# Kernel optimization log

Hardware: AMD Instinct MI355X
Metric: run time of the kernel (lower is better)

The kernel has to match this reference:

```python
import jax, jax.numpy as jnp
import numpy as np

B, M, D, H, DH = 8, 1024, 768, 12, 64
R, RF, RW, DFF = 32, 384, 384, 3072
EPS = 1e-12  # BERT LayerNorm eps


def _ln(z, g, b):
    mu = jnp.mean(z, -1, keepdims=True)
    var = jnp.mean((z - mu) ** 2, -1, keepdims=True)
    return g * (z - mu) * jax.lax.rsqrt(var + EPS) + b


def setup_inputs() -> dict:
    ks = jax.random.split(jax.random.key(0), 20)
    n = lambda k, s: jax.random.normal(k, s, dtype=jnp.float32) * 0.02
    return {
        "x": jax.random.normal(ks[0], (B, M, D), dtype=jnp.float32),
        "mask": jnp.zeros((B, M), jnp.float32),  # additive attention mask
        "Pq": n(ks[1], (H, D, R)), "Vq": n(ks[2], (H, R, DH)), "bq": n(ks[3], (H, DH)),
        "Pk": n(ks[4], (H, D, R)), "Vk": n(ks[5], (H, R, DH)), "bk": n(ks[6], (H, DH)),
        "Pv": n(ks[7], (H, D, R)), "Vv": n(ks[8], (H, R, DH)), "bv": n(ks[9], (H, DH)),
        "Uo": n(ks[10], (D, RW)), "Vo": n(ks[11], (RW, D)), "bo_attn": n(ks[12], (D,)),
        "U1": n(ks[13], (D, RF)), "V1": n(ks[14], (RF, DFF)), "b1": n(ks[15], (DFF,)),
        "U2": n(ks[16], (DFF, RF)), "V2": n(ks[17], (RF, D)), "b2": n(ks[18], (D,)),
        "ln1_g": jnp.ones((D,), jnp.float32), "ln1_b": jnp.zeros((D,), jnp.float32),
        "ln2_g": jnp.ones((D,), jnp.float32), "ln2_b": jnp.zeros((D,), jnp.float32),
    }


def reference(x, mask, Pq, Vq, bq, Pk, Vk, bk, Pv, Vv, bv, Uo, Vo, bo_attn,
              U1, V1, b1, U2, V2, b2, ln1_g, ln1_b, ln2_g, ln2_b):
    Bx, Mx, dm = x.shape
    dh = dm // Pq.shape[0]
    scale = 1.0 / (dh ** 0.5)
    # low-rank per-head Q/K/V: x @ P (d->r) then @ V (r->dh), + per-head bias
    Q = jnp.einsum('bmd,hdr,hrk->bhmk', x, Pq, Vq) + bq[None, :, None, :]
    K = jnp.einsum('bmd,hdr,hrk->bhmk', x, Pk, Vk) + bk[None, :, None, :]
    V = jnp.einsum('bmd,hdr,hrk->bhmk', x, Pv, Vv) + bv[None, :, None, :]
    scores = jnp.einsum('bhmk,bhnk->bhmn', Q, K) * scale + mask[:, None, None, :]
    probs = jax.nn.softmax(scores, axis=-1)
    attn = jnp.einsum('bhmn,bhnk->bhmk', probs, V)
    attn = attn.transpose(0, 2, 1, 3).reshape(Bx, Mx, dm)  # (B, M, d_model)
    # low-rank attention output projection + residual + LN1
    x1 = _ln(x + (attn @ Uo) @ Vo + bo_attn, ln1_g, ln1_b)
    # low-rank FFN: GELU((x1 @ U1) @ V1 + b1) @ U2 @ V2 + b2 (BERT exact gelu)
    mid = x1 @ U1
    y = (jax.nn.gelu(mid @ V1 + b1, approximate=False) @ U2) @ V2 + b2
    return _ln(x1 + y, ln2_g, ln2_b)
```

## Files before the change

kernel.cpp:

```cpp
#include <hip/hip_runtime.h>
#include <cstddef>

#define D_MODEL 768
#define NHEAD   12
#define DHEAD   64
#define RANK    32
#define SEQ     1024
#define BATCH   8
#define BM      8192

typedef __attribute__((ext_vector_type(8))) short short8;
typedef __attribute__((ext_vector_type(4))) float floatx4;

__device__ inline ushort f2b(float f) {
  union { float f; unsigned u; } v; v.f = f;
  unsigned r = v.u + 0x7fffu + ((v.u >> 16) & 1u);
  return (ushort)(r >> 16);
}
__device__ inline float b2f(ushort h) {
  union { unsigned u; float f; } v; v.u = ((unsigned)h) << 16;
  return v.f;
}
__device__ inline unsigned pk2(float a, float b) {
  return ((__float_as_uint(b) + 0x8000u) & 0xffff0000u) |
         ((__float_as_uint(a) + 0x8000u) >> 16);
}
__device__ inline float fast_gelu(float x) {
  float z = 0.79788456080286536f * (x + 0.044715f * x * x * x);
  float e = __expf(2.f * z);
  float t = 1.f - 2.f / (e + 1.f);
  return 0.5f * x * (1.f + t);
}

__global__ __launch_bounds__(256) void f2b_kernel(
    const float* __restrict__ in, ushort* __restrict__ out, int n) {
  int i = (blockIdx.x * 256 + threadIdx.x) * 4;
  if (i >= n) return;
  float4 v = *(const float4*)(in + i);
  ushort4 o;
  o.x = f2b(v.x); o.y = f2b(v.y); o.z = f2b(v.z); o.w = f2b(v.w);
  *(ushort4*)(out + i) = o;
}

__global__ __launch_bounds__(256) void combine_qkv_kernel(
    const float* __restrict__ Pq, const float* __restrict__ Vq,
    const float* __restrict__ Pk, const float* __restrict__ Vk,
    const float* __restrict__ Pv, const float* __restrict__ Vv,
    ushort* __restrict__ Wt) {
  int which = blockIdx.y;
  const float* P  = which == 0 ? Pq : (which == 1 ? Pk : Pv);
  const float* Vw = which == 0 ? Vq : (which == 1 ? Vk : Vv);
  ushort* W = Wt + (size_t)which * D_MODEL * D_MODEL;
  int idx = blockIdx.x * 256 + threadIdx.x;
  if (idx >= D_MODEL * NHEAD * DHEAD) return;
  int c = idx / D_MODEL;
  int d = idx - c * D_MODEL;
  int h = c >> 6, k = c & 63;
  const float* p = P + ((size_t)h * D_MODEL + d) * RANK;
  const float* v = Vw + (size_t)h * RANK * DHEAD + k;
  float s = 0.f;
#pragma unroll
  for (int r = 0; r < RANK; r++) s += p[r] * v[(size_t)r * DHEAD];
  W[(size_t)c * D_MODEL + d] = f2b(s);
}

__global__ __launch_bounds__(256) void concat_bias_kernel(
    const float* __restrict__ bq, const float* __restrict__ bk,
    const float* __restrict__ bv, float* __restrict__ out) {
  int i = blockIdx.x * 256 + threadIdx.x;
  if (i >= 2304) return;
  out[i] = (i < 768) ? bq[i] : (i < 1536 ? bk[i - 768] : bv[i - 1536]);
}

__global__ __launch_bounds__(256) void prep_weights_kernel(
    const float* __restrict__ U1, const float* __restrict__ V1,
    const float* __restrict__ U2, const float* __restrict__ V2,
    const float* __restrict__ Vo, const float* __restrict__ Uo,
    ushort* __restrict__ U1t, ushort* __restrict__ V1t,
    ushort* __restrict__ U2t, ushort* __restrict__ V2t,
    ushort* __restrict__ VoT, ushort* __restrict__ Uob) {
  __shared__ float t[32][33];
  int blk = blockIdx.x;
  if (blk >= 3168) {
    int i = (blk - 3168) * 1024 + threadIdx.x * 4;
    float4 v = *(const float4*)(Uo + i);
    ushort4 o;
    o.x = f2b(v.x); o.y = f2b(v.y); o.z = f2b(v.z); o.w = f2b(v.w);
    *(ushort4*)(Uob + i) = o;
    return;
  }
  const float* in; ushort* out; int R, C, bx, by;
  if (blk < 288)       { in = U1; out = U1t; R = 768;  C = 384;  int i = blk;        bx = i % 12; by = i / 12; }
  else if (blk < 1440) { in = V1; out = V1t; R = 384;  C = 3072; int i = blk - 288;  bx = i % 96; by = i / 96; }
  else if (blk < 2592) { in = U2; out = U2t; R = 3072; C = 384;  int i = blk - 1440; bx = i % 12; by = i / 12; }
  else if (blk < 2880) { in = V2; out = V2t; R = 384;  C = 768;  int i = blk - 2592; bx = i % 24; by = i / 24; }
  else                 { in = Vo; out = VoT; R = 384;  C = 768;  int i = blk - 2880; bx = i % 24; by = i / 24; }
  int c0 = bx * 32, r0 = by * 32;
  int lx = threadIdx.x & 31, ly = threadIdx.x >> 5;
#pragma unroll
  for (int i = 0; i < 32; i += 8)
    t[ly + i][lx] = in[(size_t)(r0 + ly + i) * C + c0 + lx];
  __syncthreads();
#pragma unroll
  for (int i = 0; i < 32; i += 8)
    out[(size_t)(c0 + ly + i) * R + r0 + lx] = f2b(t[lx][ly + i]);
}

template <int OUTMODE, int BIAS, int GELU>
__global__ __launch_bounds__(256) void gemm_mfma_kernel(
    const ushort* __restrict__ A, const ushort* __restrict__ Bt,
    const float* __restrict__ bias, void* __restrict__ C,
    void* __restrict__ C2, void* __restrict__ C3,
    int M, int N, int K) {
  __shared__ __align__(16) ushort Als[128 * 32];
  __shared__ __align__(16) ushort Bls[128 * 32];
  const int tid  = threadIdx.x;
  const int lane = tid & 63;
  const int quad = lane >> 4, l16 = lane & 15;
  const int wu   = __builtin_amdgcn_readfirstlane(tid >> 6);
  const int wrow = (wu >> 1) * 64, wcol = (wu & 1) * 64;
  const int row0 = blockIdx.x * 128, col0 = blockIdx.y * 128;

  floatx4 acc[4][4] = {};

  for (int k0 = 0; k0 < K; k0 += 32) {
    __syncthreads();
#pragma unroll
    for (int is = 0; is < 2; is++) {
      int c = is * 256 + wu * 64 + lane;
      int m = c >> 2, kk = (c & 3) << 3;
      const ushort* ga = A + (size_t)(row0 + m) * K + (k0 + kk);
      ushort* la = Als + (size_t)(is * 256 + wu * 64) * 8;
      __builtin_amdgcn_global_load_lds(
          (const __attribute__((address_space(1))) void*)ga,
          (__attribute__((address_space(3))) void*)la, 16, 0, 0);
      const ushort* gb = Bt + (size_t)(col0 + m) * K + (k0 + kk);
      ushort* lb = Bls + (size_t)(is * 256 + wu * 64) * 8;
      __builtin_amdgcn_global_load_lds(
          (const __attribute__((address_space(1))) void*)gb,
          (__attribute__((address_space(3))) void*)lb, 16, 0, 0);
    }
    __syncthreads();

    short8 af[4], bf[4];
#pragma unroll
    for (int mt = 0; mt < 4; mt++)
      af[mt] = *(const short8*)(Als + ((wrow + mt * 16 + l16) * 32 + quad * 8));
#pragma unroll
    for (int nt = 0; nt < 4; nt++)
      bf[nt] = *(const short8*)(Bls + ((wcol + nt * 16 + l16) * 32 + quad * 8));
#pragma unroll
    for (int mt = 0; mt < 4; mt++)
#pragma unroll
      for (int nt = 0; nt < 4; nt++)
        acc[mt][nt] = __builtin_amdgcn_mfma_f32_16x16x32_bf16(
            af[mt], bf[nt], acc[mt][nt], 0, 0, 0);
  }

#pragma unroll
  for (int mt = 0; mt < 4; mt++) {
#pragma unroll
    for (int nt = 0; nt < 4; nt++) {
      int colg = col0 + wcol + nt * 16 + l16;
      float bv_ = BIAS ? bias[colg] : 0.f;
      float v4[4];
#pragma unroll
      for (int r = 0; r < 4; r++) {
        float v = acc[mt][nt][r] + bv_;
        if (GELU) v = fast_gelu(v);
        v4[r] = v;
      }
      int rowg0 = row0 + wrow + mt * 16 + quad * 4;
      if (OUTMODE == 3) {
        int seg = col0 / 768;
        int cl = colg - seg * 768;
        if (seg == 2) {
          ushort4 o;
          o.x = f2b(v4[0]); o.y = f2b(v4[1]); o.z = f2b(v4[2]); o.w = f2b(v4[3]);
          *(ushort4*)((ushort*)C3 + (size_t)cl * BM + rowg0) = o;
        } else {
          ushort* dst = (seg == 0) ? (ushort*)C : (ushort*)C2;
          float sc = (seg == 0) ? 0.125f : 1.f;
#pragma unroll
          for (int r = 0; r < 4; r++)
            dst[(size_t)(rowg0 + r) * D_MODEL + cl] = f2b(v4[r] * sc);
        }
      } else {
#pragma unroll
        for (int r = 0; r < 4; r++)
          ((ushort*)C)[(size_t)(rowg0 + r) * N + colg] = f2b(v4[r]);
      }
    }
  }
}

template <int BIAS>
__global__ __launch_bounds__(256) void gemm_n64_kernel(
    const ushort* __restrict__ A, const ushort* __restrict__ Bt,
    const float* __restrict__ bias, ushort* __restrict__ C,
    int M, int N, int K) {
  __shared__ __align__(16) ushort Als[128 * 32];
  __shared__ __align__(16) ushort Bls[64 * 32];
  const int tid  = threadIdx.x;
  const int lane = tid & 63;
  const int quad = lane >> 4, l16 = lane & 15;
  const int wu   = __builtin_amdgcn_readfirstlane(tid >> 6);
  const int row0 = blockIdx.x * 128, col0 = blockIdx.y * 64;

  floatx4 acc[2][4] = {};

  for (int k0 = 0; k0 < K; k0 += 32) {
    __syncthreads();
#pragma unroll
    for (int is = 0; is < 2; is++) {
      int c = is * 256 + wu * 64 + lane;
      int m = c >> 2, kk = (c & 3) << 3;
      const ushort* ga = A + (size_t)(row0 + m) * K + (k0 + kk);
      ushort* la = Als + (size_t)(is * 256 + wu * 64) * 8;
      __builtin_amdgcn_global_load_lds(
          (const __attribute__((address_space(1))) void*)ga,
          (__attribute__((address_space(3))) void*)la, 16, 0, 0);
    }
    {
      int c = wu * 64 + lane;
      int m = c >> 2, kk = (c & 3) << 3;
      const ushort* gb = Bt + (size_t)(col0 + m) * K + (k0 + kk);
      ushort* lb = Bls + (size_t)(wu * 64) * 8;
      __builtin_amdgcn_global_load_lds(
          (const __attribute__((address_space(1))) void*)gb,
          (__attribute__((address_space(3))) void*)lb, 16, 0, 0);
    }
    __syncthreads();

    short8 af[2], bf[4];
#pragma unroll
    for (int mt = 0; mt < 2; mt++)
      af[mt] = *(const short8*)(Als + ((wu * 32 + mt * 16 + l16) * 32 + quad * 8));
#pragma unroll
    for (int nt = 0; nt < 4; nt++)
      bf[nt] = *(const short8*)(Bls + ((nt * 16 + l16) * 32 + quad * 8));
#pragma unroll
    for (int mt = 0; mt < 2; mt++)
#pragma unroll
      for (int nt = 0; nt < 4; nt++)
        acc[mt][nt] = __builtin_amdgcn_mfma_f32_16x16x32_bf16(
            af[mt], bf[nt], acc[mt][nt], 0, 0, 0);
  }

#pragma unroll
  for (int mt = 0; mt < 2; mt++) {
#pragma unroll
    for (int nt = 0; nt < 4; nt++) {
      int colg = col0 + nt * 16 + l16;
      float bv_ = BIAS ? bias[colg] : 0.f;
      int rowg0 = row0 + wu * 32 + mt * 16 + quad * 4;
#pragma unroll
      for (int r = 0; r < 4; r++)
        C[(size_t)(rowg0 + r) * N + colg] = f2b(acc[mt][nt][r] + bv_);
    }
  }
}

__global__ __launch_bounds__(256) void gemm_mfma_splitk_kernel(
    const ushort* __restrict__ A, const ushort* __restrict__ Bt,
    float* __restrict__ Cpart, int M, int N, int Ktot, int Kper) {
  __shared__ __align__(16) ushort Als[128 * 32];
  __shared__ __align__(16) ushort Bls[128 * 32];
  const int tid  = threadIdx.x;
  const int lane = tid & 63;
  const int quad = lane >> 4, l16 = lane & 15;
  const int wu   = __builtin_amdgcn_readfirstlane(tid >> 6);
  const int wrow = (wu >> 1) * 64, wcol = (wu & 1) * 64;
  const int row0 = blockIdx.x * 128, col0 = blockIdx.y * 128;
  const int kbase = blockIdx.z * Kper;
  float* Cz = Cpart + (size_t)blockIdx.z * M * N;

  floatx4 acc[4][4] = {};

  for (int k0 = kbase; k0 < kbase + Kper; k0 += 32) {
    __syncthreads();
#pragma unroll
    for (int is = 0; is < 2; is++) {
      int c = is * 256 + wu * 64 + lane;
      int m = c >> 2, kk = (c & 3) << 3;
      const ushort* ga = A + (size_t)(row0 + m) * Ktot + (k0 + kk);
      ushort* la = Als + (size_t)(is * 256 + wu * 64) * 8;
      __builtin_amdgcn_global_load_lds(
          (const __attribute__((address_space(1))) void*)ga,
          (__attribute__((address_space(3))) void*)la, 16, 0, 0);
      const ushort* gb = Bt + (size_t)(col0 + m) * Ktot + (k0 + kk);
      ushort* lb = Bls + (size_t)(is * 256 + wu * 64) * 8;
      __builtin_amdgcn_global_load_lds(
          (const __attribute__((address_space(1))) void*)gb,
          (__attribute__((address_space(3))) void*)lb, 16, 0, 0);
    }
    __syncthreads();

    short8 af[4], bf[4];
#pragma unroll
    for (int mt = 0; mt < 4; mt++)
      af[mt] = *(const short8*)(Als + ((wrow + mt * 16 + l16) * 32 + quad * 8));
#pragma unroll
    for (int nt = 0; nt < 4; nt++)
      bf[nt] = *(const short8*)(Bls + ((wcol + nt * 16 + l16) * 32 + quad * 8));
#pragma unroll
    for (int mt = 0; mt < 4; mt++)
#pragma unroll
      for (int nt = 0; nt < 4; nt++)
        acc[mt][nt] = __builtin_amdgcn_mfma_f32_16x16x32_bf16(
            af[mt], bf[nt], acc[mt][nt], 0, 0, 0);
  }

#pragma unroll
  for (int mt = 0; mt < 4; mt++)
#pragma unroll
    for (int nt = 0; nt < 4; nt++) {
      int colg = col0 + wcol + nt * 16 + l16;
      int rowg0 = row0 + wrow + mt * 16 + quad * 4;
#pragma unroll
      for (int r = 0; r < 4; r++)
        Cz[(size_t)(rowg0 + r) * N + colg] = acc[mt][nt][r];
    }
}

__global__ __launch_bounds__(256) void reduce_splitk_kernel(
    const float* __restrict__ part, ushort* __restrict__ out, int n, int S) {
  int i = (blockIdx.x * 256 + threadIdx.x) * 4;
  if (i >= n) return;
  float4 a = *(const float4*)(part + i);
  for (int s = 1; s < S; s++) {
    float4 b = *(const float4*)(part + (size_t)s * n + i);
    a.x += b.x; a.y += b.y; a.z += b.z; a.w += b.w;
  }
  ushort4 o;
  o.x = f2b(a.x); o.y = f2b(a.y); o.z = f2b(a.z); o.w = f2b(a.w);
  *(ushort4*)(out + i) = o;
}

__global__ __launch_bounds__(256, 3) void attn_mfma_kernel(
    const ushort* __restrict__ Q, const ushort* __restrict__ K,
    const ushort* __restrict__ Vt, const float* __restrict__ mask,
    ushort* __restrict__ O) {
  const int bid  = blockIdx.x;
  const int xcd  = bid & 7;
  const int rest = bid >> 3;
  const int qt   = rest & 7;
  const int grp  = (rest >> 3) * 8 + xcd;
  const int h = grp % 12, b = grp / 12;

  const int tid = threadIdx.x;
  const int lane = tid & 63;
  const int quad = lane >> 4, l16 = lane & 15;
  const int wu = __builtin_amdgcn_readfirstlane(tid >> 6);
  const int qrow0 = qt * 128 + wu * 32;

  __shared__ __align__(16) ushort Ks[2][64 * 64];
  __shared__ __align__(16) ushort Vts[2][64 * 64];
  __shared__ __align__(16) float Msk[SEQ];

  *(float4*)(Msk + tid * 4) = *(const float4*)(mask + (size_t)b * SEQ + tid * 4);

  short8 qf[2][2];
#pragma unroll
  for (int rt = 0; rt < 2; rt++) {
    const ushort* qp = Q + ((size_t)(b * SEQ + qrow0 + rt * 16 + l16)) * D_MODEL
                     + h * DHEAD + quad * 8;
    qf[rt][0] = *(const short8*)qp;
    qf[rt][1] = *(const short8*)(qp + 32);
  }

  const int j0 = tid >> 3, ck = tid & 7;
  const ushort* Kg = K + ((size_t)(b * SEQ + j0)) * D_MODEL + h * DHEAD + ck * 8;
  const ushort* Vg = Vt + ((size_t)(h * DHEAD + j0)) * BM + b * SEQ + ck * 8;
  const int kloff = j0 * 64 + ((ck ^ (j0 & 7)) << 3);

  short8 kst[2], vst[2];
#pragma unroll
  for (int p = 0; p < 2; p++) {
    kst[p] = *(const short8*)(Kg + (size_t)(p * 32) * D_MODEL);
    vst[p] = *(const short8*)(Vg + (size_t)p * (32 * BM));
  }
#pragma unroll
  for (int p = 0; p < 2; p++) {
    *(short8*)(&Ks[0][0] + kloff + p * (32 * 64)) = kst[p];
    *(short8*)(&Vts[0][0] + kloff + p * (32 * 64)) = vst[p];
  }
#pragma unroll
  for (int p = 0; p < 2; p++) {
    kst[p] = *(const short8*)(Kg + (size_t)(64 + p * 32) * D_MODEL);
    vst[p] = *(const short8*)(Vg + 64 + (size_t)p * (32 * BM));
  }
  asm volatile("s_waitcnt lgkmcnt(0)" ::: "memory");
  __builtin_amdgcn_s_barrier();
  asm volatile("" ::: "memory");

  float lsum[2] = {0.f, 0.f};
  floatx4 o_acc[2][4] = {};

  for (int n0 = 0; n0 < SEQ; n0 += 64) {
    const int cur = (n0 >> 6) & 1;

    if (n0 + 64 < SEQ) {
#pragma unroll
      for (int p = 0; p < 2; p++) {
        *(short8*)(&Ks[cur ^ 1][0] + kloff + p * (32 * 64)) = kst[p];
        *(short8*)(&Vts[cur ^ 1][0] + kloff + p * (32 * 64)) = vst[p];
      }
      if (n0 + 128 < SEQ) {
#pragma unroll
        for (int p = 0; p < 2; p++) {
          kst[p] = *(const short8*)(Kg + (size_t)(n0 + 128 + p * 32) * D_MODEL);
          vst[p] = *(const short8*)(Vg + (n0 + 128) + (size_t)p * (32 * BM));
        }
      }
    }

    __builtin_amdgcn_s_setprio(1);
    unsigned UA[2][4], UB[2][4];
#pragma unroll
    for (int ct = 0; ct < 4; ct++) {
      int krow = ct * 16 + l16;
      int sa = (quad ^ (l16 & 7)) << 3;
      const ushort* kbp = &Ks[cur][0] + krow * 64;
      short8 ka = *(const short8*)(kbp + sa);
      short8 kb = *(const short8*)(kbp + (sa ^ 32));
      float4 mk = *(const float4*)(Msk + n0 + ct * 16 + quad * 4);
#pragma unroll
      for (int rt = 0; rt < 2; rt++) {
        floatx4 st = {};
        st = __builtin_amdgcn_mfma_f32_16x16x32_bf16(ka, qf[rt][0], st, 0, 0, 0);
        st = __builtin_amdgcn_mfma_f32_16x16x32_bf16(kb, qf[rt][1], st, 0, 0, 0);
        float e0 = __expf(st[0] + mk.x);
        float e1 = __expf(st[1] + mk.y);
        float e2 = __expf(st[2] + mk.z);
        float e3 = __expf(st[3] + mk.w);
        lsum[rt] += (e0 + e1) + (e2 + e3);
        UA[rt][ct] = pk2(e0, e1);
        UB[rt][ct] = pk2(e2, e3);
      }
    }

#pragma unroll
    for (int kk = 0; kk < 2; kk++) {
      short8 pa[2];
#pragma unroll
      for (int rt = 0; rt < 2; rt++) {
        unsigned a0 = UA[rt][2 * kk], a2 = UA[rt][2 * kk + 1];
        unsigned b1 = UB[rt][2 * kk], b3 = UB[rt][2 * kk + 1];
        asm("v_permlane32_swap_b32 %0, %1" : "+v"(a0), "+v"(a2));
        asm("v_permlane16_swap_b32 %0, %1" : "+v"(a0), "+v"(a2));
        asm("v_permlane32_swap_b32 %0, %1" : "+v"(b1), "+v"(b3));
        asm("v_permlane16_swap_b32 %0, %1" : "+v"(b1), "+v"(b3));
        int4 t;
        t.x = (int)a0;
        t.y = (int)b1;
        t.z = (int)a2;
        t.w = (int)b3;
        pa[rt] = *(short8*)&t;
      }
#pragma unroll
      for (int dt = 0; dt < 4; dt++) {
        int vr = dt * 16 + l16;
        short8 vb = *(const short8*)(&Vts[cur][0] + vr * 64
                                     + (((kk * 4 + quad) ^ (l16 & 7)) << 3));
#pragma unroll
        for (int rt = 0; rt < 2; rt++)
          o_acc[rt][dt] = __builtin_amdgcn_mfma_f32_16x16x32_bf16(
              pa[rt], vb, o_acc[rt][dt], 0, 0, 0);
      }
    }
    __builtin_amdgcn_s_setprio(0);

    if (n0 + 64 < SEQ) {
      asm volatile("s_waitcnt lgkmcnt(0)" ::: "memory");
      __builtin_amdgcn_s_barrier();
      asm volatile("" ::: "memory");
    }
  }

#pragma unroll
  for (int rt = 0; rt < 2; rt++) {
    float l = lsum[rt];
    l += __shfl_xor(l, 16);
    l += __shfl_xor(l, 32);
    float inv = 1.f / l;
    int lanebase = lane & 48;
#pragma unroll
    for (int rr = 0; rr < 4; rr++) {
      int iv = __builtin_amdgcn_ds_bpermute((lanebase | (quad * 4 + rr)) << 2,
                                            __float_as_int(inv));
      float invr = __int_as_float(iv);
      size_t rowg = (size_t)(b * SEQ + qrow0 + rt * 16 + quad * 4 + rr);
#pragma unroll
      for (int dt = 0; dt < 4; dt++)
        O[rowg * D_MODEL + h * DHEAD + dt * 16 + l16] = f2b(o_acc[rt][dt][rr] * invr);
    }
  }
}

template <int AIN_BF16, int OUT_FP32, int OUT_BF16>
__global__ __launch_bounds__(256) void add_ln_kernel(
    const float* __restrict__ Ainf, const ushort* __restrict__ Ainb,
    const ushort* __restrict__ Binb,
    const float* __restrict__ g, const float* __restrict__ bt,
    float* __restrict__ outf, ushort* __restrict__ outb) {
  const int row = blockIdx.x, tid = threadIdx.x;
  __shared__ float red[4];
  float v[3];
  float s = 0.f;
#pragma unroll
  for (int u = 0; u < 3; u++) {
    int c = tid + u * 256;
    float a = AIN_BF16 ? b2f(Ainb[(size_t)row * 768 + c]) : Ainf[(size_t)row * 768 + c];
    v[u] = a + b2f(Binb[(size_t)row * 768 + c]);
    s += v[u];
  }
#pragma unroll
  for (int off = 32; off > 0; off >>= 1) s += __shfl_down(s, off);
  if ((tid & 63) == 0) red[tid >> 6] = s;
  __syncthreads();
  float mu = (red[0] + red[1] + red[2] + red[3]) * (1.f / 768.f);
  float s2 = 0.f;
#pragma unroll
  for (int u = 0; u < 3; u++) { float d = v[u] - mu; s2 += d * d; }
#pragma unroll
  for (int off = 32; off > 0; off >>= 1) s2 += __shfl_down(s2, off);
  __syncthreads();
  if ((tid & 63) == 0) red[tid >> 6] = s2;
  __syncthreads();
  float var = (red[0] + red[1] + red[2] + red[3]) * (1.f / 768.f);
  float inv = rsqrtf(var + 1e-12f);
#pragma unroll
  for (int u = 0; u < 3; u++) {
    int c = tid + u * 256;
    float r = g[c] * (v[u] - mu) * inv + bt[c];
    if (OUT_FP32) outf[(size_t)row * 768 + c] = r;
    if (OUT_BF16) outb[(size_t)row * 768 + c] = f2b(r);
  }
}

extern "C" void kernel_launch(void* const* d_in, const int* in_sizes, int n_in,
                              void* d_out, int out_size, void* d_ws, size_t ws_size,
                              hipStream_t stream) {
  const float* x    = (const float*)d_in[0];
  const float* mask = (const float*)d_in[1];
  const float* Pq   = (const float*)d_in[2];
  const float* Vq   = (const float*)d_in[3];
  const float* bq   = (const float*)d_in[4];
  const float* Pk   = (const float*)d_in[5];
  const float* Vk   = (const float*)d_in[6];
  const float* bk   = (const float*)d_in[7];
  const float* Pv   = (const float*)d_in[8];
  const float* Vv   = (const float*)d_in[9];
  const float* bv   = (const float*)d_in[10];
  const float* Uo   = (const float*)d_in[11];
  const float* Vo   = (const float*)d_in[12];
  const float* bo   = (const float*)d_in[13];
  const float* U1   = (const float*)d_in[14];
  const float* V1   = (const float*)d_in[15];
  const float* b1   = (const float*)d_in[16];
  const float* U2   = (const float*)d_in[17];
  const float* V2   = (const float*)d_in[18];
  const float* b2   = (const float*)d_in[19];
  const float* g1   = (const float*)d_in[20];
  const float* be1  = (const float*)d_in[21];
  const float* g2   = (const float*)d_in[22];
  const float* be2  = (const float*)d_in[23];

  char* w = (char*)d_ws;
  auto alloc = [&](size_t bytes) -> char* {
    char* p = w; w += (bytes + 255) & ~(size_t)255; return p;
  };
  ushort* xb     = (ushort*)alloc((size_t)BM * 768 * 2);
  ushort* Wqkvt  = (ushort*)alloc((size_t)2304 * 768 * 2);
  float*  ball   = (float*)alloc(2304 * 4);
  ushort* VoT    = (ushort*)alloc(768 * 384 * 2);
  ushort* Uob    = (ushort*)alloc(768 * 384 * 2);
  ushort* Wot    = (ushort*)alloc(768 * 768 * 2);
  ushort* U1t    = (ushort*)alloc(384 * 768 * 2);
  ushort* V1t    = (ushort*)alloc((size_t)3072 * 384 * 2);
  ushort* U2t    = (ushort*)alloc((size_t)384 * 3072 * 2);
  ushort* V2t    = (ushort*)alloc(768 * 384 * 2);
  ushort* Qb     = (ushort*)alloc((size_t)BM * 768 * 2);
  ushort* Kb     = (ushort*)alloc((size_t)BM * 768 * 2);
  ushort* Vtb    = (ushort*)alloc((size_t)768 * BM * 2);
  ushort* attnb  = (ushort*)alloc((size_t)BM * 768 * 2);
  ushort* mtb    = (ushort*)alloc((size_t)BM * 384 * 2);
  ushort* y1b    = (ushort*)alloc((size_t)BM * 768 * 2);
  ushort* x1b    = (ushort*)alloc((size_t)BM * 768 * 2);
  float*  part   = (float*)alloc((size_t)4 * BM * 384 * 4);
  ushort* hiddenb = Qb;
  ushort* y2b     = y1b;
  float*  outp    = (float*)d_out;

  f2b_kernel<<<(BM * 768) / 1024, 256, 0, stream>>>(x, xb, BM * 768);
  combine_qkv_kernel<<<dim3(2304, 3), 256, 0, stream>>>(Pq, Vq, Pk, Vk, Pv, Vv, Wqkvt);
  concat_bias_kernel<<<9, 256, 0, stream>>>(bq, bk, bv, ball);
  prep_weights_kernel<<<3456, 256, 0, stream>>>(U1, V1, U2, V2, Vo, Uo,
                                                U1t, V1t, U2t, V2t, VoT, Uob);
  gemm_n64_kernel<0><<<dim3(6, 12), 256, 0, stream>>>(VoT, Uob, nullptr, Wot, 768, 768, 384);

  gemm_mfma_kernel<3, 1, 0><<<dim3(64, 18), 256, 0, stream>>>(
      xb, Wqkvt, ball, Qb, Kb, Vtb, BM, 2304, 768);

  attn_mfma_kernel<<<dim3(768), 256, 0, stream>>>(Qb, Kb, Vtb, mask, attnb);

  gemm_n64_kernel<1><<<dim3(64, 12), 256, 0, stream>>>(attnb, Wot, bo, y1b, BM, 768, 768);
  add_ln_kernel<0, 0, 1><<<BM, 256, 0, stream>>>(x, nullptr, y1b, g1, be1, nullptr, x1b);

  gemm_n64_kernel<0><<<dim3(64, 6), 256, 0, stream>>>(
      x1b, U1t, nullptr, mtb, BM, 384, 768);
  gemm_mfma_kernel<1, 1, 1><<<dim3(64, 24), 256, 0, stream>>>(
      mtb, V1t, b1, hiddenb, nullptr, nullptr, BM, 3072, 384);
  gemm_mfma_splitk_kernel<<<dim3(64, 3, 2), 256, 0, stream>>>(
      hiddenb, U2t, part, BM, 384, 3072, 1536);
  reduce_splitk_kernel<<<(BM * 384) / 1024, 256, 0, stream>>>(part, mtb, BM * 384, 2);
  gemm_n64_kernel<1><<<dim3(64, 12), 256, 0, stream>>>(mtb, V2t, b2, y2b, BM, 768, 384);

  add_ln_kernel<1, 1, 0><<<BM, 256, 0, stream>>>(nullptr, x1b, y2b, g2, be2, outp, nullptr);
}
```

Baseline: 413.1 us.

## Double-buffer the MFMA GEMM with register prefetch and swizzled LDS, reuse it for projections

The main 128x128 MFMA GEMM now uses a K-step of 64 with two LDS buffers. The next tile is loaded from global into registers while the current tile is computed, and the LDS layout is XOR-swizzled to avoid bank conflicts. This removes one barrier per step and the exposed load latency, and adds setprio around the MFMA block. The output-projection, U1 and V2 GEMMs are switched from the n64 kernel to this kernel with half as many blocks. The cost is more LDS (64KB per block), higher register pressure, and fewer blocks for the narrow GEMMs.

```diff
diff --git a/kernel.cpp b/kernel.cpp
--- a/kernel.cpp
+++ b/kernel.cpp
@@ -107,13 +107,13 @@
 }
 
 template <int OUTMODE, int BIAS, int GELU>
-__global__ __launch_bounds__(256) void gemm_mfma_kernel(
+__global__ __launch_bounds__(256, 2) void gemm_mfma_kernel(
     const ushort* __restrict__ A, const ushort* __restrict__ Bt,
     const float* __restrict__ bias, void* __restrict__ C,
     void* __restrict__ C2, void* __restrict__ C3,
     int M, int N, int K) {
-  __shared__ __align__(16) ushort Als[128 * 32];
-  __shared__ __align__(16) ushort Bls[128 * 32];
+  __shared__ __align__(16) ushort Als[2][128 * 64];
+  __shared__ __align__(16) ushort Bls[2][128 * 64];
   const int tid  = threadIdx.x;
   const int lane = tid & 63;
   const int quad = lane >> 4, l16 = lane & 15;
@@ -121,40 +121,84 @@
   const int wrow = (wu >> 1) * 64, wcol = (wu & 1) * 64;
   const int row0 = blockIdx.x * 128, col0 = blockIdx.y * 128;
 
+  const int r_ = tid >> 3, sl_ = tid & 7;
+  const ushort* Ag = A + (size_t)(row0 + r_) * K + sl_ * 8;
+  const ushort* Bg = Bt + (size_t)(col0 + r_) * K + sl_ * 8;
+  const int loff = r_ * 64 + ((sl_ ^ (r_ & 7)) << 3);
+
+  const int nsteps = K >> 6;
+  short8 ast[4], bst[4];
+
+#pragma unroll
+  for (int p = 0; p < 4; p++) {
+    ast[p] = *(const short8*)(Ag + (size_t)(32 * p) * K);
+    bst[p] = *(const short8*)(Bg + (size_t)(32 * p) * K);
+  }
+#pragma unroll
+  for (int p = 0; p < 4; p++) {
+    *(short8*)(&Als[0][0] + loff + p * (32 * 64)) = ast[p];
+    *(short8*)(&Bls[0][0] + loff + p * (32 * 64)) = bst[p];
+  }
+#pragma unroll
+  for (int p = 0; p < 4; p++) {
+    ast[p] = *(const short8*)(Ag + (size_t)(32 * p) * K + 64);
+    bst[p] = *(const short8*)(Bg + (size_t)(32 * p) * K + 64);
+  }
+  asm volatile("s_waitcnt lgkmcnt(0)" ::: "memory");
+  __builtin_amdgcn_s_barrier();
+  asm volatile("" ::: "memory");
+
   floatx4 acc[4][4] = {};
 
-  for (int k0 = 0; k0 < K; k0 += 32) {
-    __syncthreads();
-#pragma unroll
-    for (int is = 0; is < 2; is++) {
-      int c = is * 256 + wu * 64 + lane;
-      int m = c >> 2, kk = (c & 3) << 3;
-      const ushort* ga = A + (size_t)(row0 + m) * K + (k0 + kk);
-      ushort* la = Als + (size_t)(is * 256 + wu * 64) * 8;
-      __builtin_amdgcn_global_load_lds(
-          (const __attribute__((address_space(1))) void*)ga,
-          (__attribute__((address_space(3))) void*)la, 16, 0, 0);
-      const ushort* gb = Bt + (size_t)(col0 + m) * K + (k0 + kk);
-      ushort* lb = Bls + (size_t)(is * 256 + wu * 64) * 8;
-      __builtin_amdgcn_global_load_lds(
-          (const __attribute__((address_space(1))) void*)gb,
-          (__attribute__((address_space(3))) void*)lb, 16, 0, 0);
-    }
-    __syncthreads();
-
-    short8 af[4], bf[4];
-#pragma unroll
-    for (int mt = 0; mt < 4; mt++)
-      af[mt] = *(const short8*)(Als + ((wrow + mt * 16 + l16) * 32 + quad * 8));
-#pragma unroll
-    for (int nt = 0; nt < 4; nt++)
-      bf[nt] = *(const short8*)(Bls + ((wcol + nt * 16 + l16) * 32 + quad * 8));
-#pragma unroll
-    for (int mt = 0; mt < 4; mt++)
-#pragma unroll
-      for (int nt = 0; nt < 4; nt++)
-        acc[mt][nt] = __builtin_amdgcn_mfma_f32_16x16x32_bf16(
-            af[mt], bf[nt], acc[mt][nt], 0, 0, 0);
+  for (int s = 0; s < nsteps; s++) {
+    const int cur = s & 1;
+
+    if (s + 1 < nsteps) {
+#pragma unroll
+      for (int p = 0; p < 4; p++) {
+        *(short8*)(&Als[cur ^ 1][0] + loff + p * (32 * 64)) = ast[p];
+        *(short8*)(&Bls[cur ^ 1][0] + loff + p * (32 * 64)) = bst[p];
+      }
+      if (s + 2 < nsteps) {
+        const int ko = (s + 2) * 64;
+#pragma unroll
+        for (int p = 0; p < 4; p++) {
+          ast[p] = *(const short8*)(Ag + (size_t)(32 * p) * K + ko);
+          bst[p] = *(const short8*)(Bg + (size_t)(32 * p) * K + ko);
+        }
+      }
+    }
+
+    __builtin_amdgcn_s_setprio(1);
+#pragma unroll
+    for (int kk = 0; kk < 2; kk++) {
+      short8 af[4], bf[4];
+#pragma unroll
+      for (int mt = 0; mt < 4; mt++) {
+        int row = wrow + mt * 16 + l16;
+        af[mt] = *(const short8*)(&Als[cur][0] + row * 64
+                                  + (((kk * 4 + quad) ^ (l16 & 7)) << 3));
+      }
+#pragma unroll
+      for (int nt = 0; nt < 4; nt++) {
+        int row = wcol + nt * 16 + l16;
+        bf[nt] = *(const short8*)(&Bls[cur][0] + row * 64
+                                  + (((kk * 4 + quad) ^ (l16 & 7)) << 3));
+      }
+#pragma unroll
+      for (int mt = 0; mt < 4; mt++)
+#pragma unroll
+        for (int nt = 0; nt < 4; nt++)
+          acc[mt][nt] = __builtin_amdgcn_mfma_f32_16x16x32_bf16(
+              af[mt], bf[nt], acc[mt][nt], 0, 0, 0);
+    }
+    __builtin_amdgcn_s_setprio(0);
+
+    if (s + 1 < nsteps) {
+      asm volatile("s_waitcnt lgkmcnt(0)" ::: "memory");
+      __builtin_amdgcn_s_barrier();
+      asm volatile("" ::: "memory");
+    }
   }
 
 #pragma unroll
@@ -605,17 +649,19 @@
 
   attn_mfma_kernel<<<dim3(768), 256, 0, stream>>>(Qb, Kb, Vtb, mask, attnb);
 
-  gemm_n64_kernel<1><<<dim3(64, 12), 256, 0, stream>>>(attnb, Wot, bo, y1b, BM, 768, 768);
+  gemm_mfma_kernel<1, 1, 0><<<dim3(64, 6), 256, 0, stream>>>(
+      attnb, Wot, bo, y1b, nullptr, nullptr, BM, 768, 768);
   add_ln_kernel<0, 0, 1><<<BM, 256, 0, stream>>>(x, nullptr, y1b, g1, be1, nullptr, x1b);
 
-  gemm_n64_kernel<0><<<dim3(64, 6), 256, 0, stream>>>(
-      x1b, U1t, nullptr, mtb, BM, 384, 768);
+  gemm_mfma_kernel<1, 0, 0><<<dim3(64, 3), 256, 0, stream>>>(
+      x1b, U1t, nullptr, mtb, nullptr, nullptr, BM, 384, 768);
   gemm_mfma_kernel<1, 1, 1><<<dim3(64, 24), 256, 0, stream>>>(
       mtb, V1t, b1, hiddenb, nullptr, nullptr, BM, 3072, 384);
   gemm_mfma_splitk_kernel<<<dim3(64, 3, 2), 256, 0, stream>>>(
       hiddenb, U2t, part, BM, 384, 3072, 1536);
   reduce_splitk_kernel<<<(BM * 384) / 1024, 256, 0, stream>>>(part, mtb, BM * 384, 2);
-  gemm_n64_kernel<1><<<dim3(64, 12), 256, 0, stream>>>(mtb, V2t, b2, y2b, BM, 768, 384);
+  gemm_mfma_kernel<1, 1, 0><<<dim3(64, 6), 256, 0, stream>>>(
+      mtb, V2t, b2, y2b, nullptr, nullptr, BM, 768, 384);
 
   add_ln_kernel<1, 1, 0><<<BM, 256, 0, stream>>>(nullptr, x1b, y2b, g2, be2, outp, nullptr);
 }
```

Measured after the change: 403.8 us. -2.2%, faster.
